# Optimization experiments

Hardware: AMD Instinct MI355X
Metric: run time of the kernel (lower is better)

Reference implementation:

```python
import jax, jax.numpy as jnp
import numpy as np

N_NODES = 100000
N_EDGES = 1600000
N_GRAPHS = 64
D = 128


def gcn_conv(x, W, b, src, dst, num_nodes):
    # PyG GCNConv: x' = D^{-1/2} (A + I) D^{-1/2} (X W) + b
    h = x @ W  # [N, H]
    deg = jax.ops.segment_sum(jnp.ones_like(dst, dtype=h.dtype), dst,
                              num_segments=num_nodes)  # includes self-loop (>=1)
    dinv = jax.lax.rsqrt(deg)
    norm = dinv[src] * dinv[dst]  # [E+N]
    msg = h[src] * norm[:, None]  # gather + scale
    out = jax.ops.segment_sum(msg, dst, num_segments=num_nodes)
    return out + b


def setup_inputs() -> dict:
    key = jax.random.key(0)
    ks = jax.random.split(key, 10)
    x = jax.random.normal(ks[0], (N_NODES, D), dtype=jnp.float32)
    edge_index = jax.random.randint(ks[1], (2, N_EDGES), 0, N_NODES, dtype=jnp.int64)
    batch = jnp.sort(jax.random.randint(ks[2], (N_NODES,), 0, N_GRAPHS, dtype=jnp.int64))
    s = 1.0 / np.sqrt(D)
    W1 = jax.random.normal(ks[3], (D, D), dtype=jnp.float32) * s
    b1 = jnp.zeros((D,), dtype=jnp.float32)
    W2 = jax.random.normal(ks[4], (D, D), dtype=jnp.float32) * s
    b2 = jnp.zeros((D,), dtype=jnp.float32)
    Wfc = jax.random.normal(ks[5], (D, D), dtype=jnp.float32) * s
    bfc = jnp.zeros((D,), dtype=jnp.float32)
    return {"x": x, "edge_index": edge_index, "batch": batch,
            "W1": W1, "b1": b1, "W2": W2, "b2": b2, "Wfc": Wfc, "bfc": bfc}


def reference(x, edge_index, batch, W1, b1, W2, b2, Wfc, bfc):
    num_nodes = x.shape[0]
    # add self-loops (PyG default add_self_loops=True)
    loop = jnp.arange(num_nodes, dtype=edge_index.dtype)
    src = jnp.concatenate([edge_index[0], loop])
    dst = jnp.concatenate([edge_index[1], loop])

    h = jax.nn.relu(gcn_conv(x, W1, b1, src, dst, num_nodes))
    h = jax.nn.relu(gcn_conv(h, W2, b2, src, dst, num_nodes))

    # global_mean_pool over graph segment ids
    sums = jax.ops.segment_sum(h, batch, num_segments=N_GRAPHS)
    cnts = jax.ops.segment_sum(jnp.ones((num_nodes,), h.dtype), batch,
                               num_segments=N_GRAPHS)
    pooled = sums / jnp.maximum(cnts, 1.0)[:, None]

    return jax.nn.relu(pooled @ Wfc + bfc)
```

## Files before the change

kernel.cpp:

```cpp
#include <hip/hip_runtime.h>
#include <hip/hip_bf16.h>
#include <stdint.h>

typedef unsigned int uint;
typedef unsigned short ushort;
typedef __attribute__((ext_vector_type(8))) short short8;
typedef __attribute__((ext_vector_type(4))) float floatx4;

#define DD 128
#define BSHIFT 9
#define NBLK 256
#define CAP 10240

__device__ __forceinline__ float bf2f(ushort h){ return __uint_as_float(((uint)h)<<16); }
__device__ __forceinline__ ushort f2bf(float f){
    uint u = __float_as_uint(f);
    u += 0x7fffu + ((u>>16)&1u);
    return (ushort)(u>>16);
}

__global__ __launch_bounds__(256) void k_canon2(
    const int* __restrict__ ei, const ushort* __restrict__ xs,
    const void* W1, const void* W2, const void* Wfc,
    const void* b1, const void* b2, const void* bfc,
    float* Wcf, float* bc1, float* bc2, float* bcf,
    ushort* wb1, ushort* wb2,
    int* flags, float* pooled, int* bukcnt, int nbuk, int PM)
{
    __shared__ int s_flg[3];
    int t = threadIdx.x, b = blockIdx.x;
    if (t < 64){
        unsigned long long m0 = __ballot((t < 32) ? (ei[2*t+1] == 0) : 1);
        uint ex2 = (((uint)xs[2*t]) >> 7) & 0xffu;
        uint ew2 = (((uint)((const ushort*)W1)[2*t]) >> 7) & 0xffu;
        unsigned long long m1 = __ballot(ex2 >= 90u && ex2 <= 160u);
        unsigned long long m2 = __ballot(ew2 >= 90u && ew2 <= 160u);
        if (t == 0){
            s_flg[0] = (m0 == ~0ull) ? 1 : 0;
            s_flg[1] = (__popcll(m1) >= 48) ? 1 : 0;
            s_flg[2] = (__popcll(m2) >= 48) ? 1 : 0;
            if (b == 0){ flags[0]=s_flg[0]; flags[1]=s_flg[1]; flags[2]=s_flg[2]; }
        }
    }
    __syncthreads();
    int fW = s_flg[2];

    int gi = b*256 + t;
    if (gi < 32768){
        int r = gi >> 14, off = gi & 16383;
        const void* s = (r==0) ? W1 : W2;
        float val = fW ? bf2f(((const ushort*)s)[off]) : ((const float*)s)[off];
        int k = off>>7, n = off&127;
        int c = n>>4, nn = n&15, kk = k>>5, q = (k>>3)&3, j = k&7;
        ushort* wb = (r==0) ? wb1 : wb2;
        wb[((c*4+kk)*64 + q*16 + nn)*8 + j] = f2bf(val);
    } else if (gi < 49152){
        int off = gi - 32768;
        Wcf[off] = fW ? bf2f(((const ushort*)Wfc)[off]) : ((const float*)Wfc)[off];
    } else if (gi < 49536){
        int jj = gi - 49152; int r = jj>>7, off = jj & 127;
        const void* s = (r==0)?b1:((r==1)?b2:bfc);
        float* d = (r==0)?bc1:((r==1)?bc2:bcf);
        d[off] = fW ? bf2f(((const ushort*)s)[off]) : ((const float*)s)[off];
    } else if (gi < 49536 + PM){
        pooled[gi - 49536] = 0.f;
    } else if (gi < 49536 + PM + nbuk){
        bukcnt[gi - 49536 - PM] = 0;
    }
}

__global__ __launch_bounds__(256) void k_scatA(const int* __restrict__ ei,
                                               int* __restrict__ bukcnt,
                                               uint* __restrict__ pairs,
                                               int E, int nbuk, int chunk){
    __shared__ int lh[256], lcur[256];
    __shared__ int s_flg;
    int t = threadIdx.x, b = blockIdx.x;
    if (t < 64){
        unsigned long long m0 = __ballot((t < 32) ? (ei[2*t+1] == 0) : 1);
        if (t == 0) s_flg = (m0 == ~0ull) ? 1 : 0;
    }
    for (int i=t;i<nbuk;i+=256) lh[i]=0;
    __syncthreads();
    int f64 = s_flg;
    int e0 = b*chunk, e1 = min(E, e0+chunk);

    {
        int e = e0 + t;
        for (; e + 768 < e1; e += 1024){
            int d0 = f64 ? ei[2*(E+e)]     : ei[E+e];
            int d1 = f64 ? ei[2*(E+e+256)] : ei[E+e+256];
            int d2 = f64 ? ei[2*(E+e+512)] : ei[E+e+512];
            int d3 = f64 ? ei[2*(E+e+768)] : ei[E+e+768];
            atomicAdd(&lh[d0>>BSHIFT], 1);
            atomicAdd(&lh[d1>>BSHIFT], 1);
            atomicAdd(&lh[d2>>BSHIFT], 1);
            atomicAdd(&lh[d3>>BSHIFT], 1);
        }
        for (; e < e1; e += 256){
            int d = f64 ? ei[2*(E+e)] : ei[E+e];
            atomicAdd(&lh[d>>BSHIFT], 1);
        }
    }
    __syncthreads();
    for (int i=t;i<nbuk;i+=256){
        int v = lh[i];
        int base = v ? atomicAdd(&bukcnt[i], v) : 0;
        lcur[i] = i*CAP + base;
    }
    __syncthreads();

    {
        int e = e0 + t;
        for (; e + 768 < e1; e += 1024){
            int d0 = f64 ? ei[2*(E+e)]     : ei[E+e];
            int d1 = f64 ? ei[2*(E+e+256)] : ei[E+e+256];
            int d2 = f64 ? ei[2*(E+e+512)] : ei[E+e+512];
            int d3 = f64 ? ei[2*(E+e+768)] : ei[E+e+768];
            int s0 = f64 ? ei[2*e]         : ei[e];
            int s1 = f64 ? ei[2*(e+256)]   : ei[e+256];
            int s2 = f64 ? ei[2*(e+512)]   : ei[e+512];
            int s3 = f64 ? ei[2*(e+768)]   : ei[e+768];
            int p0 = atomicAdd(&lcur[d0>>BSHIFT], 1);
            int p1 = atomicAdd(&lcur[d1>>BSHIFT], 1);
            int p2 = atomicAdd(&lcur[d2>>BSHIFT], 1);
            int p3 = atomicAdd(&lcur[d3>>BSHIFT], 1);
            pairs[p0] = (uint)s0 | ((uint)(d0 & 511) << 23);
            pairs[p1] = (uint)s1 | ((uint)(d1 & 511) << 23);
            pairs[p2] = (uint)s2 | ((uint)(d2 & 511) << 23);
            pairs[p3] = (uint)s3 | ((uint)(d3 & 511) << 23);
        }
        for (; e < e1; e += 256){
            int d = f64 ? ei[2*(E+e)] : ei[E+e];
            int s = f64 ? ei[2*e]     : ei[e];
            int p = atomicAdd(&lcur[d>>BSHIFT], 1);
            pairs[p] = (uint)s | ((uint)(d & 511) << 23);
        }
    }
}

__global__ __launch_bounds__(256) void k_build(const uint* __restrict__ pairs,
                                               const int* __restrict__ bukcnt,
                                               int* __restrict__ rowstart,
                                               int* __restrict__ rowend,
                                               float* __restrict__ dinv,
                                               int* __restrict__ srcb,
                                               int nbuk, int M){
    __shared__ int cnt[512], off[512], cur[512], ps[256];
    int b = blockIdx.x, t = threadIdx.x;
    int base = b*CAP;
    int m = bukcnt[b];
    for (int i=t;i<512;i+=256) cnt[i]=0;
    __syncthreads();
    for (int e=t; e<m; e+=256){
        uint pr = pairs[base+e];
        atomicAdd(&cnt[pr >> 23], 1);
    }
    __syncthreads();
    int c0 = cnt[2*t], c1 = cnt[2*t+1];
    int s = c0 + c1;
    ps[t] = s; __syncthreads();
    for (int o2=1; o2<256; o2<<=1){
        int x = (t>=o2) ? ps[t-o2] : 0;
        __syncthreads(); ps[t] += x; __syncthreads();
    }
    int ex = ps[t] - s;
    off[2*t] = ex;     off[2*t+1] = ex + c0;
    cur[2*t] = ex;     cur[2*t+1] = ex + c0;
    __syncthreads();
    for (int i=t;i<512;i+=256){
        int n = (b<<BSHIFT) + i;
        if (n < M){
            rowstart[n] = base + off[i];
            rowend[n]   = base + off[i] + cnt[i];
            dinv[n]     = rsqrtf((float)(cnt[i]+1));
        }
    }
    for (int e=t; e<m; e+=256){
        uint pr = pairs[base+e];
        int i = pr >> 23;
        int p = atomicAdd(&cur[i], 1);
        srcb[base+p] = (int)(pr & 0x7FFFFFu);
    }
}

__global__ __launch_bounds__(256) void k_gemm(const ushort* __restrict__ Xb,
                                              const float* __restrict__ Xf,
                                              const ushort* __restrict__ Wb,
                                              const float* __restrict__ dinv,
                                              const int* __restrict__ flags, int force_bf16,
                                              ushort* __restrict__ Hp, int M){
    __shared__ uint4 Ws4[2048];
    int t = threadIdx.x;
    int n0 = blockIdx.x*64;
    int xbf = force_bf16 ? 1 : flags[1];

    {
        const uint4* sW = (const uint4*)Wb;
        #pragma unroll
        for (int j=0;j<8;j++) Ws4[t + j*256] = sW[t + j*256];
    }

    int wv = t>>6, lane = t&63;
    int mrow = lane & 15, q = lane >> 4;
    int arow = n0 + wv*16 + mrow;
    int rok  = (arow < M);

    short8 af[4];
    if (xbf){
        const ushort* xr = Xb + (size_t)arow*DD + q*8;
        #pragma unroll
        for (int kk=0;kk<4;kk++){
            uint4 v = rok ? *(const uint4*)(xr + kk*32) : make_uint4(0,0,0,0);
            af[kk] = *(const short8*)&v;
        }
    } else {
        const float* xr = Xf + (size_t)arow*DD + q*8;
        #pragma unroll
        for (int kk=0;kk<4;kk++){
            float4 a = make_float4(0,0,0,0), b4 = make_float4(0,0,0,0);
            if (rok){
                a  = *(const float4*)(xr + kk*32);
                b4 = *(const float4*)(xr + kk*32 + 4);
            }
            uint4 v;
            v.x = (uint)f2bf(a.x)  | ((uint)f2bf(a.y)<<16);
            v.y = (uint)f2bf(a.z)  | ((uint)f2bf(a.w)<<16);
            v.z = (uint)f2bf(b4.x) | ((uint)f2bf(b4.y)<<16);
            v.w = (uint)f2bf(b4.z) | ((uint)f2bf(b4.w)<<16);
            af[kk] = *(const short8*)&v;
        }
    }
    __syncthreads();

    const ushort* Ws = (const ushort*)Ws4;
    floatx4 acc[8];
    #pragma unroll
    for (int c=0;c<8;c++) acc[c] = (floatx4){0.f,0.f,0.f,0.f};

    #pragma unroll
    for (int kk=0;kk<4;kk++){
        #pragma unroll
        for (int c=0;c<8;c++){
            short8 bf = *(const short8*)(Ws + ((size_t)((c*4+kk)*64 + lane))*8);
            acc[c] = __builtin_amdgcn_mfma_f32_16x16x32_bf16(af[kk], bf, acc[c], 0, 0, 0);
        }
    }

    int quad = lane>>4, col = lane&15;
    int rbase = n0 + wv*16 + quad*4;
    float dv[4];
    #pragma unroll
    for (int r=0;r<4;r++) dv[r] = (rbase + r < M) ? dinv[rbase + r] : 0.f;
    #pragma unroll
    for (int c=0;c<8;c++){
        #pragma unroll
        for (int r=0;r<4;r++){
            int gn = rbase + r;
            if (gn < M) Hp[(size_t)gn*DD + c*16 + col] = f2bf(acc[c][r]*dv[r]);
        }
    }
}

__global__ __launch_bounds__(256) void k_gather(const ushort* __restrict__ Hp,
                                                const int* __restrict__ rowstart,
                                                const int* __restrict__ rowend,
                                                const int* __restrict__ srcb,
                                                const float* __restrict__ dinv,
                                                const float* __restrict__ bc,
                                                ushort* __restrict__ Xout, int M){
    int wid  = (int)((blockIdx.x*(size_t)blockDim.x + threadIdx.x) >> 6);
    int lane = threadIdx.x & 63;
    if (wid >= M) return;
    int q   = lane >> 4;
    int l16 = lane & 15;
    const uint4* Hp4 = (const uint4*)Hp;

    float acc[8];
    #pragma unroll
    for (int c=0;c<8;c++) acc[c] = 0.f;

    #define ACCUM(vv) { \
        acc[0] += __uint_as_float((vv).x<<16); acc[1] += __uint_as_float((vv).x&0xffff0000u); \
        acc[2] += __uint_as_float((vv).y<<16); acc[3] += __uint_as_float((vv).y&0xffff0000u); \
        acc[4] += __uint_as_float((vv).z<<16); acc[5] += __uint_as_float((vv).z&0xffff0000u); \
        acc[6] += __uint_as_float((vv).w<<16); acc[7] += __uint_as_float((vv).w&0xffff0000u); }

    int rp  = rowstart[wid];
    int rp1 = rowend[wid];
    int total = (rp1 - rp) + 1;
    int j = 0;
    while (j < total){
        int m = total - j; if (m > 64) m = 64;
        int pos = j + lane;
        int idx = wid;
        if (lane < m && pos > 0) idx = srcb[rp + pos - 1];
        for (int g = 0; g < m; g += 8){
            int r0 = g + q, r1 = g + 4 + q;
            int s0 = __shfl(idx, r0, 64);
            int s1 = __shfl(idx, r1, 64);
            uint4 v0 = make_uint4(0,0,0,0), v1 = make_uint4(0,0,0,0);
            if (r0 < m) v0 = Hp4[(size_t)s0*16 + l16];
            if (r1 < m) v1 = Hp4[(size_t)s1*16 + l16];
            ACCUM(v0);
            ACCUM(v1);
        }
        j += m;
    }
    #undef ACCUM

    #pragma unroll
    for (int c=0;c<8;c++){
        acc[c] += __shfl_xor(acc[c], 16, 64);
        acc[c] += __shfl_xor(acc[c], 32, 64);
    }

    if (lane < 16){
        float w = dinv[wid];
        const float* bp = bc + l16*8;
        uint4 o;
        float r0,r1;
        r0 = fmaxf(fmaf(acc[0], w, bp[0]), 0.f);
        r1 = fmaxf(fmaf(acc[1], w, bp[1]), 0.f);
        o.x = (uint)f2bf(r0) | ((uint)f2bf(r1)<<16);
        r0 = fmaxf(fmaf(acc[2], w, bp[2]), 0.f);
        r1 = fmaxf(fmaf(acc[3], w, bp[3]), 0.f);
        o.y = (uint)f2bf(r0) | ((uint)f2bf(r1)<<16);
        r0 = fmaxf(fmaf(acc[4], w, bp[4]), 0.f);
        r1 = fmaxf(fmaf(acc[5], w, bp[5]), 0.f);
        o.z = (uint)f2bf(r0) | ((uint)f2bf(r1)<<16);
        r0 = fmaxf(fmaf(acc[6], w, bp[6]), 0.f);
        r1 = fmaxf(fmaf(acc[7], w, bp[7]), 0.f);
        o.w = (uint)f2bf(r0) | ((uint)f2bf(r1)<<16);
        ((uint4*)Xout)[(size_t)wid*16 + l16] = o;
    }
}

__global__ __launch_bounds__(256) void k_pool(const ushort* __restrict__ X3,
                                              const int* __restrict__ batch,
                                              const int* __restrict__ flags,
                                              float* __restrict__ pooled, int M){
    int f = flags[0];
    int t = threadIdx.x;
    int c32 = t & 63;
    int row = t >> 6;
    int n0 = blockIdx.x * 256;
    if (n0 >= M) return;
    int nend = n0 + 256; if (nend > M) nend = M;
    const uint* X3u = (const uint*)X3;

    float a0 = 0.f, a1 = 0.f;
    int cur = -1;

    int n = n0 + row;
    #define POOL_PROC(gg, uu) \
        if ((gg) != cur){ \
            if (cur >= 0){ \
                atomicAdd(&pooled[cur*DD + 2*c32],   a0); \
                atomicAdd(&pooled[cur*DD + 2*c32+1], a1); \
            } \
            a0 = 0.f; a1 = 0.f; cur = (gg); \
        } \
        a0 += __uint_as_float((uu)<<16); \
        a1 += __uint_as_float((uu) & 0xffff0000u);

    for (; n + 12 < nend; n += 16){
        int g0 = f ? batch[2*n]      : batch[n];
        int g1 = f ? batch[2*(n+4)]  : batch[n+4];
        int g2 = f ? batch[2*(n+8)]  : batch[n+8];
        int g3 = f ? batch[2*(n+12)] : batch[n+12];
        uint u0 = X3u[(size_t)n*64      + c32];
        uint u1 = X3u[(size_t)(n+4)*64  + c32];
        uint u2 = X3u[(size_t)(n+8)*64  + c32];
        uint u3 = X3u[(size_t)(n+12)*64 + c32];
        POOL_PROC(g0, u0);
        POOL_PROC(g1, u1);
        POOL_PROC(g2, u2);
        POOL_PROC(g3, u3);
    }
    for (; n < nend; n += 4){
        int g = f ? batch[2*n] : batch[n];
        uint u = X3u[(size_t)n*64 + c32];
        POOL_PROC(g, u);
    }
    #undef POOL_PROC

    if (cur >= 0){
        atomicAdd(&pooled[cur*DD + 2*c32],   a0);
        atomicAdd(&pooled[cur*DD + 2*c32+1], a1);
    }
}

__global__ void k_fc(const float* __restrict__ pooled, const int* __restrict__ batch,
                     const int* __restrict__ flags,
                     const float* __restrict__ Wcf, const float* __restrict__ bcf,
                     ushort* out16, float* out32, int M){
    __shared__ float p[128];
    __shared__ int sb[2];
    int g = blockIdx.x, t = threadIdx.x;
    int f = flags[0];
    if (t < 2){
        int target = g - t;
        int lo = 0, hi = M;
        while (lo < hi){ int mid=(lo+hi)>>1; int bv = f ? batch[2*mid] : batch[mid]; if (bv > target) hi = mid; else lo = mid+1; }
        sb[t] = lo;
    }
    __syncthreads();
    float cnt = (float)(sb[0] - sb[1]);
    p[t] = pooled[g*DD + t] / fmaxf(cnt, 1.f);
    __syncthreads();
    float acc = bcf[t];
    #pragma unroll 8
    for (int k=0;k<128;k++) acc = fmaf(p[k], Wcf[k*DD + t], acc);
    float r = fmaxf(acc, 0.f);
    if (flags[1]) out16[g*DD + t] = f2bf(r);
    else          out32[g*DD + t] = r;
}

extern "C" void kernel_launch(void* const* d_in, const int* in_sizes, int n_in,
                              void* d_out, int out_size, void* d_ws, size_t ws_size,
                              hipStream_t stream) {
    const ushort* xs  = (const ushort*)d_in[0];
    const float*  xf  = (const float*)d_in[0];
    const int*    ei  = (const int*)d_in[1];
    const int*    bat = (const int*)d_in[2];
    const void* W1  = d_in[3];
    const void* b1  = d_in[4];
    const void* W2  = d_in[5];
    const void* b2  = d_in[6];
    const void* Wfc = d_in[7];
    const void* bfc = d_in[8];

    int M = in_sizes[0] / DD;
    int E = in_sizes[1] / 2;
    int G = out_size / DD;
    int nbuk  = (M + 511) >> BSHIFT;
    int chunk = (E + NBLK - 1) / NBLK;

    char* w = (char*)d_ws;
    auto alloc = [&](size_t bytes)->void*{ void* p = (void*)w; w += (bytes + 255) & ~(size_t)255; return p; };
    int*    flags    = (int*)   alloc(16);
    int*    rowstart = (int*)   alloc((size_t)M*4);
    int*    rowend   = (int*)   alloc((size_t)M*4);
    int*    bukcnt   = (int*)   alloc((size_t)nbuk*4);
    float*  dinv     = (float*) alloc((size_t)M*4);
    float*  pooled   = (float*) alloc((size_t)G*DD*4);
    float*  Wcf      = (float*) alloc(16384*4);
    float*  bc1      = (float*) alloc(128*4);
    float*  bc2      = (float*) alloc(128*4);
    float*  bcf      = (float*) alloc(128*4);
    ushort* wb1      = (ushort*)alloc(16384*2);
    ushort* wb2      = (ushort*)alloc(16384*2);
    int*    srcb     = (int*)   alloc((size_t)nbuk*CAP*4);
    ushort* Hp       = (ushort*)alloc((size_t)M*DD*2);
    ushort* X2       = (ushort*)alloc((size_t)M*DD*2);
    uint*   pairs    = (uint*)Hp;
    (void)ws_size; (void)n_in;

    int PM = G*DD;
    int canon_n = 49536 + PM + nbuk;

    k_canon2<<<(canon_n+255)/256, 256, 0, stream>>>(ei, xs, W1, W2, Wfc, b1, b2, bfc,
                                                    Wcf, bc1, bc2, bcf, wb1, wb2,
                                                    flags, pooled, bukcnt, nbuk, PM);
    k_scatA <<<NBLK, 256, 0, stream>>>(ei, bukcnt, pairs, E, nbuk, chunk);
    k_build <<<nbuk, 256, 0, stream>>>(pairs, bukcnt, rowstart, rowend, dinv, srcb, nbuk, M);

    k_gemm  <<<(M+63)/64, 256, 0, stream>>>(xs, xf, wb1, dinv, flags, 0, Hp, M);
    k_gather<<<(M+3)/4, 256, 0, stream>>>(Hp, rowstart, rowend, srcb, dinv, bc1, X2, M);
    k_gemm  <<<(M+63)/64, 256, 0, stream>>>(X2, (const float*)X2, wb2, dinv, flags, 1, Hp, M);
    k_gather<<<(M+3)/4, 256, 0, stream>>>(Hp, rowstart, rowend, srcb, dinv, bc2, X2, M);

    k_pool<<<(M+255)/256, 256, 0, stream>>>(X2, bat, flags, pooled, M);
    k_fc  <<<G, 128, 0, stream>>>(pooled, bat, flags, Wcf, bcf, (ushort*)d_out, (float*)d_out, M);
}
```

Baseline: 320.7 us.

## Cache dst indices in registers in scatter and stage GEMM output through LDS

The edge-bucketing kernel now keeps each thread's destination indices in a fixed-size register array, so the second pass no longer re-reads them from global memory. The grid is sized so each thread handles at most 32 edges. The GEMM epilogue writes bf16 results into shared memory first and then stores full 16-byte rows to global memory instead of scattered 2-byte stores. This trades extra register pressure and a shared-memory round trip for fewer and more coalesced global accesses.

```diff
diff --git a/kernel.cpp b/kernel.cpp
--- a/kernel.cpp
+++ b/kernel.cpp
@@ -9,8 +9,8 @@
 
 #define DD 128
 #define BSHIFT 9
-#define NBLK 256
 #define CAP 10240
+#define MAXIT 32
 
 __device__ __forceinline__ float bf2f(ushort h){ return __uint_as_float(((uint)h)<<16); }
 __device__ __forceinline__ ushort f2bf(float f){
@@ -85,20 +85,13 @@
     int f64 = s_flg;
     int e0 = b*chunk, e1 = min(E, e0+chunk);
 
-    {
-        int e = e0 + t;
-        for (; e + 768 < e1; e += 1024){
-            int d0 = f64 ? ei[2*(E+e)]     : ei[E+e];
-            int d1 = f64 ? ei[2*(E+e+256)] : ei[E+e+256];
-            int d2 = f64 ? ei[2*(E+e+512)] : ei[E+e+512];
-            int d3 = f64 ? ei[2*(E+e+768)] : ei[E+e+768];
-            atomicAdd(&lh[d0>>BSHIFT], 1);
-            atomicAdd(&lh[d1>>BSHIFT], 1);
-            atomicAdd(&lh[d2>>BSHIFT], 1);
-            atomicAdd(&lh[d3>>BSHIFT], 1);
-        }
-        for (; e < e1; e += 256){
+    int dc[MAXIT];
+    #pragma unroll
+    for (int k=0;k<MAXIT;k++){
+        int e = e0 + t + k*256;
+        if (e < e1){
             int d = f64 ? ei[2*(E+e)] : ei[E+e];
+            dc[k] = d;
             atomicAdd(&lh[d>>BSHIFT], 1);
         }
     }
@@ -109,30 +102,12 @@
         lcur[i] = i*CAP + base;
     }
     __syncthreads();
-
-    {
-        int e = e0 + t;
-        for (; e + 768 < e1; e += 1024){
-            int d0 = f64 ? ei[2*(E+e)]     : ei[E+e];
-            int d1 = f64 ? ei[2*(E+e+256)] : ei[E+e+256];
-            int d2 = f64 ? ei[2*(E+e+512)] : ei[E+e+512];
-            int d3 = f64 ? ei[2*(E+e+768)] : ei[E+e+768];
-            int s0 = f64 ? ei[2*e]         : ei[e];
-            int s1 = f64 ? ei[2*(e+256)]   : ei[e+256];
-            int s2 = f64 ? ei[2*(e+512)]   : ei[e+512];
-            int s3 = f64 ? ei[2*(e+768)]   : ei[e+768];
-            int p0 = atomicAdd(&lcur[d0>>BSHIFT], 1);
-            int p1 = atomicAdd(&lcur[d1>>BSHIFT], 1);
-            int p2 = atomicAdd(&lcur[d2>>BSHIFT], 1);
-            int p3 = atomicAdd(&lcur[d3>>BSHIFT], 1);
-            pairs[p0] = (uint)s0 | ((uint)(d0 & 511) << 23);
-            pairs[p1] = (uint)s1 | ((uint)(d1 & 511) << 23);
-            pairs[p2] = (uint)s2 | ((uint)(d2 & 511) << 23);
-            pairs[p3] = (uint)s3 | ((uint)(d3 & 511) << 23);
-        }
-        for (; e < e1; e += 256){
-            int d = f64 ? ei[2*(E+e)] : ei[E+e];
-            int s = f64 ? ei[2*e]     : ei[e];
+    #pragma unroll
+    for (int k=0;k<MAXIT;k++){
+        int e = e0 + t + k*256;
+        if (e < e1){
+            int d = dc[k];
+            int s = f64 ? ei[2*e] : ei[e];
             int p = atomicAdd(&lcur[d>>BSHIFT], 1);
             pairs[p] = (uint)s | ((uint)(d & 511) << 23);
         }
@@ -247,18 +222,28 @@
         }
     }
 
+    __syncthreads();
     int quad = lane>>4, col = lane&15;
     int rbase = n0 + wv*16 + quad*4;
     float dv[4];
     #pragma unroll
     for (int r=0;r<4;r++) dv[r] = (rbase + r < M) ? dinv[rbase + r] : 0.f;
+
+    ushort* eb = (ushort*)Ws4 + (size_t)wv * 16*136;
     #pragma unroll
     for (int c=0;c<8;c++){
         #pragma unroll
         for (int r=0;r<4;r++){
-            int gn = rbase + r;
-            if (gn < M) Hp[(size_t)gn*DD + c*16 + col] = f2bf(acc[c][r]*dv[r]);
-        }
+            eb[(quad*4+r)*136 + c*16 + col] = f2bf(acc[c][r]*dv[r]);
+        }
+    }
+    #pragma unroll
+    for (int h=0;h<4;h++){
+        int i = lane*4 + h;
+        int row = i >> 4, u = i & 15;
+        uint4 v = *(const uint4*)(eb + row*136 + u*8);
+        int gn = n0 + wv*16 + row;
+        if (gn < M) *(uint4*)(Hp + (size_t)gn*DD + u*8) = v;
     }
 }
 
@@ -435,7 +420,8 @@
     int E = in_sizes[1] / 2;
     int G = out_size / DD;
     int nbuk  = (M + 511) >> BSHIFT;
-    int chunk = (E + NBLK - 1) / NBLK;
+    int nblkA = (E + 8191) / 8192; if (nblkA < 256) nblkA = 256;
+    int chunk = (E + nblkA - 1) / nblkA;
 
     char* w = (char*)d_ws;
     auto alloc = [&](size_t bytes)->void*{ void* p = (void*)w; w += (bytes + 255) & ~(size_t)255; return p; };
@@ -463,7 +449,7 @@
     k_canon2<<<(canon_n+255)/256, 256, 0, stream>>>(ei, xs, W1, W2, Wfc, b1, b2, bfc,
                                                     Wcf, bc1, bc2, bcf, wb1, wb2,
                                                     flags, pooled, bukcnt, nbuk, PM);
-    k_scatA <<<NBLK, 256, 0, stream>>>(ei, bukcnt, pairs, E, nbuk, chunk);
+    k_scatA <<<nblkA, 256, 0, stream>>>(ei, bukcnt, pairs, E, nbuk, chunk);
     k_build <<<nbuk, 256, 0, stream>>>(pairs, bukcnt, rowstart, rowend, dinv, srcb, nbuk, M);
 
     k_gemm  <<<(M+63)/64, 256, 0, stream>>>(xs, xf, wb1, dinv, flags, 0, Hp, M);
```

New measurement: 321.4 us. About the same (+0.2%).
